# Kernel optimization log

Hardware: AMD Instinct MI355X
Metric: run time of the kernel (lower is better)

Reference implementation:

```python
import jax, jax.numpy as jnp
import numpy as np

NB_CLUSTERS = 128   # C: number of clusters (equal-size, sorted ids)
PTS_PER_CLUSTER = 1024  # P: points per cluster
DIM = 3


def setup_inputs() -> dict:
    key = jax.random.key(0)
    k1, k2 = jax.random.split(key)
    n = NB_CLUSTERS * PTS_PER_CLUSTER
    input_points = jax.random.normal(k1, (n, DIM), dtype=jnp.float32)
    output_points = jax.random.normal(k2, (n, DIM), dtype=jnp.float32)
    clusters = jnp.repeat(jnp.arange(NB_CLUSTERS, dtype=jnp.int32), PTS_PER_CLUSTER)
    return {
        "input_points": input_points,
        "input_clusters": clusters,
        "output_points": output_points,
        "output_clusters": clusters,
    }


def reference(input_points, input_clusters, output_points, output_clusters):
    # Original: nb_clusters = max(input_clusters); loop for i in range(nb_clusters)
    # -> the HIGHEST cluster id is excluded from the loss. Reproduced via mask.
    nb = jnp.max(input_clusters)  # == NB_CLUSTERS - 1
    a = input_points.reshape(NB_CLUSTERS, PTS_PER_CLUSTER, DIM)   # [C,P,3]
    b = output_points.reshape(NB_CLUSTERS, PTS_PER_CLUSTER, DIM)  # [C,P,3]

    # Pairwise squared distances per cluster: d[c,i,j] = ||a[c,i]-b[c,j]||^2
    d = (jnp.sum(a * a, axis=-1)[:, :, None]
         + jnp.sum(b * b, axis=-1)[:, None, :]
         - 2.0 * jnp.einsum('cid,cjd->cij', a, b))  # [C,P,P]

    # Indices computed under no_grad in the original (ints: no grad anyway).
    idx1 = jnp.argmin(d, axis=2)  # for each input point: nearest output point
    idx2 = jnp.argmin(d, axis=1)  # for each output point: nearest input point

    near_b = jnp.take_along_axis(b, idx1[..., None], axis=1)  # [C,P,3]
    near_a = jnp.take_along_axis(a, idx2[..., None], axis=1)  # [C,P,3]

    l1 = jnp.sum((a - near_b) ** 2, axis=(1, 2))  # [C]
    l2 = jnp.sum((b - near_a) ** 2, axis=(1, 2))  # [C]

    mask = (jnp.arange(NB_CLUSTERS) < nb).astype(a.dtype)  # exclude last cluster
    return jnp.sum(mask * (l1 + l2))
```

## Files before the change

### kernel.cpp

```cpp
#include <hip/hip_runtime.h>


#define PTS   1024
#define ACTIVE_CLUSTERS 127
#define QHALF 512
#define QG    64
#define Q     8
#define SEG   16
#define TPB   1024
#define TSEG  (PTS / SEG)

__global__ __launch_bounds__(TPB) void chamfer_kernel(
    const float* __restrict__ pts_in,
    const float* __restrict__ pts_out,
    float* __restrict__ out)
{
    const int b    = blockIdx.x;
    const int c    = b >> 2;
    const int dir  = (b >> 1) & 1;
    const int half = b & 1;

    const float* __restrict__ query  = dir ? pts_out : pts_in;
    const float* __restrict__ target = dir ? pts_in  : pts_out;

    __shared__ __align__(16) float sx[PTS];
    __shared__ __align__(16) float sy[PTS];
    __shared__ __align__(16) float sz[PTS];
    __shared__ __align__(16) float sh[PTS];
    __shared__ unsigned colmin[QHALF];
    __shared__ float wsum[16];

    const int tid = threadIdx.x;
    const int qi  = tid & (QG - 1);
    const int seg = tid >> 6;
    const size_t base = (size_t)c * PTS * 3;

    if (tid < QHALF) colmin[tid] = 0x7f7fffffu;

    {
        const float* tp = target + base + (size_t)tid * 3;
        float x = tp[0], y = tp[1], z = tp[2];
        sx[tid] = x; sy[tid] = y; sz[tid] = z;
        sh[tid] = fmaf(x, x, fmaf(y, y, z * z));
    }

    float qx[Q], qy[Q], qz[Q], mn[Q];
    #pragma unroll
    for (int k = 0; k < Q; ++k) {
        const float* qp = query + base
                        + (size_t)(half * QHALF + k * QG + qi) * 3;
        qx[k] = -2.0f * qp[0];
        qy[k] = -2.0f * qp[1];
        qz[k] = -2.0f * qp[2];
        mn[k] = 3.4e38f;
    }
    __syncthreads();

    const int j0 = seg * TSEG;
    #pragma unroll 1
    for (int jj = 0; jj < TSEG; jj += 4) {
        const float4 bx = *(const float4*)&sx[j0 + jj];
        const float4 by = *(const float4*)&sy[j0 + jj];
        const float4 bz = *(const float4*)&sz[j0 + jj];
        const float4 bh = *(const float4*)&sh[j0 + jj];
        #pragma unroll
        for (int k = 0; k < Q; ++k) {
            float s0 = fmaf(qx[k], bx.x, fmaf(qy[k], by.x, fmaf(qz[k], bz.x, bh.x)));
            float s1 = fmaf(qx[k], bx.y, fmaf(qy[k], by.y, fmaf(qz[k], bz.y, bh.y)));
            float s2 = fmaf(qx[k], bx.z, fmaf(qy[k], by.z, fmaf(qz[k], bz.z, bh.z)));
            float s3 = fmaf(qx[k], bx.w, fmaf(qy[k], by.w, fmaf(qz[k], bz.w, bh.w)));
            mn[k] = fminf(fminf(s0, s1), mn[k]);
            mn[k] = fminf(fminf(s2, s3), mn[k]);
        }
    }

    #pragma unroll
    for (int k = 0; k < Q; ++k) {
        float n2 = fmaf(qx[k], qx[k], fmaf(qy[k], qy[k], qz[k] * qz[k]));
        float v  = fmaf(0.25f, n2, mn[k]);
        atomicMin(&colmin[k * QG + qi], __float_as_uint(v));
    }
    __syncthreads();

    float v = (tid < QHALF) ? __uint_as_float(colmin[tid]) : 0.0f;
    #pragma unroll
    for (int off = 32; off > 0; off >>= 1)
        v += __shfl_down(v, off, 64);

    const int wave = tid >> 6;
    const int lane = tid & 63;
    if (lane == 0) wsum[wave] = v;
    __syncthreads();

    if (wave == 0) {
        float t = (lane < 16) ? wsum[lane] : 0.0f;
        #pragma unroll
        for (int off = 8; off > 0; off >>= 1)
            t += __shfl_down(t, off, 64);
        if (lane == 0) atomicAdd(out, t);
    }
}

extern "C" void kernel_launch(void* const* d_in, const int* in_sizes, int n_in,
                              void* d_out, int out_size, void* d_ws, size_t ws_size,
                              hipStream_t stream) {
    const float* input_points  = (const float*)d_in[0];
    const float* output_points = (const float*)d_in[2];
    float* out = (float*)d_out;

    hipMemsetAsync(out, 0, sizeof(float), stream);

    chamfer_kernel<<<dim3(ACTIVE_CLUSTERS * 2 * 2), dim3(TPB), 0, stream>>>(
        input_points, output_points, out);
}
```

Measured before the change: 87.17 us.

## Pack target points as paired float4 to enable packed-FMA inner loop

Replaces the four structure-of-arrays shared buffers with an interleaved float4 layout holding two target points per pair (x0,x1,y0,y1 / z0,z1,h0,h1). The inner loop now handles two targets per iteration with unroll 2. The pairing appears meant to let the compiler emit packed FP32 ops (v_pk_fma_f32) on adjacent lanes, halving the instruction count of the distance evaluation. The shared-memory fill now uses half the threads, each loading six floats.

```diff
diff --git a/kernel.cpp b/kernel.cpp
--- a/kernel.cpp
+++ b/kernel.cpp
@@ -23,10 +23,7 @@
     const float* __restrict__ query  = dir ? pts_out : pts_in;
     const float* __restrict__ target = dir ? pts_in  : pts_out;
 
-    __shared__ __align__(16) float sx[PTS];
-    __shared__ __align__(16) float sy[PTS];
-    __shared__ __align__(16) float sz[PTS];
-    __shared__ __align__(16) float sh[PTS];
+    __shared__ __align__(16) float4 st4[PTS];
     __shared__ unsigned colmin[QHALF];
     __shared__ float wsum[16];
 
@@ -37,11 +34,14 @@
 
     if (tid < QHALF) colmin[tid] = 0x7f7fffffu;
 
-    {
-        const float* tp = target + base + (size_t)tid * 3;
-        float x = tp[0], y = tp[1], z = tp[2];
-        sx[tid] = x; sy[tid] = y; sz[tid] = z;
-        sh[tid] = fmaf(x, x, fmaf(y, y, z * z));
+    if (tid < PTS / 2) {
+        const float* tp = target + base + (size_t)tid * 6;
+        float x0 = tp[0], y0 = tp[1], z0 = tp[2];
+        float x1 = tp[3], y1 = tp[4], z1 = tp[5];
+        float h0 = fmaf(x0, x0, fmaf(y0, y0, z0 * z0));
+        float h1 = fmaf(x1, x1, fmaf(y1, y1, z1 * z1));
+        st4[tid * 2]     = make_float4(x0, x1, y0, y1);
+        st4[tid * 2 + 1] = make_float4(z0, z1, h0, h1);
     }
 
     float qx[Q], qy[Q], qz[Q], mn[Q];
@@ -56,21 +56,16 @@
     }
     __syncthreads();
 
-    const int j0 = seg * TSEG;
-    #pragma unroll 1
-    for (int jj = 0; jj < TSEG; jj += 4) {
-        const float4 bx = *(const float4*)&sx[j0 + jj];
-        const float4 by = *(const float4*)&sy[j0 + jj];
-        const float4 bz = *(const float4*)&sz[j0 + jj];
-        const float4 bh = *(const float4*)&sh[j0 + jj];
+    const int p0 = seg * (TSEG / 2);
+    #pragma unroll 2
+    for (int p = 0; p < TSEG / 2; ++p) {
+        const float4 c0 = st4[(p0 + p) * 2];
+        const float4 c1 = st4[(p0 + p) * 2 + 1];
         #pragma unroll
         for (int k = 0; k < Q; ++k) {
-            float s0 = fmaf(qx[k], bx.x, fmaf(qy[k], by.x, fmaf(qz[k], bz.x, bh.x)));
-            float s1 = fmaf(qx[k], bx.y, fmaf(qy[k], by.y, fmaf(qz[k], bz.y, bh.y)));
-            float s2 = fmaf(qx[k], bx.z, fmaf(qy[k], by.z, fmaf(qz[k], bz.z, bh.z)));
-            float s3 = fmaf(qx[k], bx.w, fmaf(qy[k], by.w, fmaf(qz[k], bz.w, bh.w)));
+            float s0 = fmaf(qx[k], c0.x, fmaf(qy[k], c0.z, fmaf(qz[k], c1.x, c1.z)));
+            float s1 = fmaf(qx[k], c0.y, fmaf(qy[k], c0.w, fmaf(qz[k], c1.y, c1.w)));
             mn[k] = fminf(fminf(s0, s1), mn[k]);
-            mn[k] = fminf(fminf(s2, s3), mn[k]);
         }
     }
 
```

Measured after the change: 86.20 us. About the same (-1.1%).
